# Kernel optimization log

Hardware: AMD Instinct MI355X
Metric: run time of the kernel (lower is better)

Reference implementation:

```python
import jax, jax.numpy as jnp
import numpy as np

IN_DIMS = 512
TOKEN_DIM = 512
NUM_HEADS = 1
D = TOKEN_DIM * NUM_HEADS
SCALE = TOKEN_DIM ** (-0.5)
EPS = 1e-12  # torch F.normalize default


def _l2norm(v, axis):
    n = jnp.sqrt(jnp.sum(v * v, axis=axis, keepdims=True))
    return v / jnp.maximum(n, EPS)


def setup_inputs() -> dict:
    key = jax.random.key(0)
    ks = jax.random.split(key, 10)
    B, C, H, W = 64, IN_DIMS, 28, 28
    s_in = IN_DIMS ** -0.5
    s_d = D ** -0.5
    return {
        "x": jax.random.normal(ks[0], (B, C, H, W), jnp.float32),
        "Wq": jax.random.normal(ks[1], (IN_DIMS, D), jnp.float32) * s_in,
        "bq": jax.random.normal(ks[2], (D,), jnp.float32) * 0.01,
        "Wk": jax.random.normal(ks[3], (IN_DIMS, D), jnp.float32) * s_in,
        "bk": jax.random.normal(ks[4], (D,), jnp.float32) * 0.01,
        "w_g": jax.random.normal(ks[5], (D, 1), jnp.float32),
        "Wp": jax.random.normal(ks[6], (D, D), jnp.float32) * s_d,
        "bp": jax.random.normal(ks[7], (D,), jnp.float32) * 0.01,
        "Wf": jax.random.normal(ks[8], (D, TOKEN_DIM), jnp.float32) * s_d,
        "bf": jax.random.normal(ks[9], (TOKEN_DIM,), jnp.float32) * 0.01,
    }


def reference(x, Wq, bq, Wk, bk, w_g, Wp, bp, Wf, bf):
    B, C, H, W = x.shape
    t = x.reshape(B, C, H * W).transpose(0, 2, 1)          # [B, N, C]
    query = _l2norm(t @ Wq + bq, axis=-1)                  # [B, N, D]
    k = _l2norm(t @ Wk + bk, axis=-1)                      # [B, N, D]
    attn = _l2norm((query @ w_g) * SCALE, axis=1)          # [B, N, 1], normalized over tokens
    ctx = jnp.sum(attn * query, axis=1, keepdims=True)     # [B, 1, D] global context
    out = (ctx * k) @ Wp + bp + query                      # [B, N, D]
    out = out @ Wf + bf                                    # [B, N, TOKEN_DIM]
    return out.transpose(0, 2, 1).reshape(B, -1, H, W)
```

## Files before the change

### kernel.cpp

```cpp
#include <hip/hip_runtime.h>

#define EPSN 1e-12f
#define SCALE_F 0.044194173824159216f

typedef __bf16 bf16x8 __attribute__((ext_vector_type(8)));
typedef __bf16 bf16x4 __attribute__((ext_vector_type(4)));
typedef float  f32x4  __attribute__((ext_vector_type(4)));

__global__ __launch_bounds__(256) void k_prep_t(const float* __restrict__ Wq,
                                                const float* __restrict__ Wk,
                                                __bf16* __restrict__ WqT,
                                                __bf16* __restrict__ WkT) {
  __shared__ float Tq[32][33], Tk[32][33];
  const int c0 = blockIdx.x * 32, d0 = blockIdx.y * 32;
  const int dx = threadIdx.x, cy = threadIdx.y;
  #pragma unroll
  for (int p = 0; p < 4; ++p) {
    int c = cy + p * 8;
    Tq[c][dx] = Wq[(size_t)(c0 + c) * 512 + d0 + dx];
    Tk[c][dx] = Wk[(size_t)(c0 + c) * 512 + d0 + dx];
  }
  __syncthreads();
  #pragma unroll
  for (int p = 0; p < 4; ++p) {
    int d = cy + p * 8;
    WqT[(size_t)(d0 + d) * 512 + c0 + dx] = (__bf16)Tq[dx][d];
    WkT[(size_t)(d0 + d) * 512 + c0 + dx] = (__bf16)Tk[dx][d];
  }
}

__global__ __launch_bounds__(512) void k_prep_w(const float* __restrict__ Wp,
                                                const float* __restrict__ Wf,
                                                const float* __restrict__ bp,
                                                const float* __restrict__ bfv,
                                                __bf16* __restrict__ WcT,
                                                float* __restrict__ bpf) {
  int kk = blockIdx.x;
  int d  = threadIdx.x;
  float a0 = 0.f, a1 = 0.f, a2 = 0.f, a3 = 0.f;
  for (int c = 0; c < 512; c += 4) {
    a0 = fmaf(Wp[kk * 512 + c],     Wf[(size_t)c * 512 + d],         a0);
    a1 = fmaf(Wp[kk * 512 + c + 1], Wf[(size_t)(c + 1) * 512 + d],   a1);
    a2 = fmaf(Wp[kk * 512 + c + 2], Wf[(size_t)(c + 2) * 512 + d],   a2);
    a3 = fmaf(Wp[kk * 512 + c + 3], Wf[(size_t)(c + 3) * 512 + d],   a3);
  }
  WcT[(size_t)d * 1024 + kk]       = (__bf16)((a0 + a1) + (a2 + a3));
  WcT[(size_t)d * 1024 + 512 + kk] = (__bf16)Wf[(size_t)kk * 512 + d];
  if (kk == 0) {
    float b0 = 0.f, b1 = 0.f;
    for (int c = 0; c < 512; c += 2) {
      b0 = fmaf(bp[c],     Wf[(size_t)c * 512 + d],       b0);
      b1 = fmaf(bp[c + 1], Wf[(size_t)(c + 1) * 512 + d], b1);
    }
    bpf[d] = b0 + b1 + bfv[d];
  }
}

__global__ __launch_bounds__(512) void k_qk(const float* __restrict__ x,
                                            const __bf16* __restrict__ WqT,
                                            const __bf16* __restrict__ WkT,
                                            const float* __restrict__ bq,
                                            const float* __restrict__ bk,
                                            const float* __restrict__ wg,
                                            __bf16* __restrict__ Qn,
                                            __bf16* __restrict__ Kn,
                                            float* __restrict__ g) {
  __shared__ __bf16 As0[64][40], As1[64][40];
  __shared__ float red[8][64], redG[8][64];
  __shared__ float invv[64];
  const int t = threadIdx.x;
  const int lane = t & 63, w = t >> 6;
  const int li = lane & 15, lq = lane >> 4;
  const int n0 = blockIdx.x * 64;
  const int b  = blockIdx.y;
  const int isK = blockIdx.z;
  const __bf16* Wt  = isK ? WkT : WqT;
  const float* bias = isK ? bk : bq;
  __bf16* dst       = isK ? Kn : Qn;
  const int sn = t & 63, sc4 = (t >> 6) * 4;
  const bool nv = (n0 + sn < 784);
  const float* xp = x + ((size_t)b * 512 + sc4) * 784 + n0 + sn;
  const __bf16* wp = Wt + (size_t)(w * 64 + li) * 512 + lq * 8;

  f32x4 acc[4][4] = {};
  bf16x8 bA[4], bB[4];
  float xA[4], xB[4];

  auto issueX = [&](float (&xr)[4], int ks) {
    #pragma unroll
    for (int j = 0; j < 4; ++j)
      xr[j] = nv ? xp[(size_t)(ks * 32 + j) * 784] : 0.f;
  };
  auto issueB = [&](bf16x8 (&bb)[4], int ks) {
    #pragma unroll
    for (int cb = 0; cb < 4; ++cb)
      bb[cb] = *(const bf16x8*)(wp + (size_t)cb * 8192 + ks * 32);
  };
  auto writeA = [&](__bf16 (*Asb)[40], const float (&xr)[4]) {
    bf16x4 v;
    #pragma unroll
    for (int j = 0; j < 4; ++j) v[j] = (__bf16)xr[j];
    *(bf16x4*)&Asb[sn][sc4] = v;
  };
  auto step = [&](const __bf16 (*Asb)[40], const bf16x8 (&bb)[4]) {
    bf16x8 af[4];
    #pragma unroll
    for (int rb = 0; rb < 4; ++rb)
      af[rb] = *(const bf16x8*)&Asb[rb * 16 + li][lq * 8];
    #pragma unroll
    for (int cb = 0; cb < 4; ++cb)
      #pragma unroll
      for (int rb = 0; rb < 4; ++rb)
        acc[rb][cb] = __builtin_amdgcn_mfma_f32_16x16x32_bf16(af[rb], bb[cb], acc[rb][cb], 0, 0, 0);
  };

  issueX(xA, 0); issueX(xB, 1); issueB(bA, 0);
  writeA(As0, xA);
  __syncthreads();

  #pragma unroll 1
  for (int ks = 0; ks < 14; ks += 2) {
    issueX(xA, ks + 2);
    issueB(bB, ks + 1);
    step(As0, bA);
    writeA(As1, xB);
    __syncthreads();
    issueX(xB, ks + 3);
    issueB(bA, ks + 2);
    step(As1, bB);
    writeA(As0, xA);
    __syncthreads();
  }
  issueB(bB, 15);
  step(As0, bA);
  writeA(As1, xB);
  __syncthreads();
  step(As1, bB);

  float bv[4], wv[4];
  #pragma unroll
  for (int cb = 0; cb < 4; ++cb) {
    int col = w * 64 + cb * 16 + li;
    bv[cb] = bias[col];
    wv[cb] = isK ? 0.f : wg[col];
  }
  #pragma unroll
  for (int rb = 0; rb < 4; ++rb)
    #pragma unroll
    for (int cb = 0; cb < 4; ++cb)
      #pragma unroll
      for (int j = 0; j < 4; ++j)
        acc[rb][cb][j] += bv[cb];
  #pragma unroll
  for (int rb = 0; rb < 4; ++rb)
    #pragma unroll
    for (int j = 0; j < 4; ++j) {
      float ss = 0.f, sg = 0.f;
      #pragma unroll
      for (int cb = 0; cb < 4; ++cb) {
        float v = acc[rb][cb][j];
        ss = fmaf(v, v, ss); sg = fmaf(v, wv[cb], sg);
      }
      ss += __shfl_xor(ss, 1); ss += __shfl_xor(ss, 2); ss += __shfl_xor(ss, 4); ss += __shfl_xor(ss, 8);
      sg += __shfl_xor(sg, 1); sg += __shfl_xor(sg, 2); sg += __shfl_xor(sg, 4); sg += __shfl_xor(sg, 8);
      if (li == 0) {
        int row = rb * 16 + lq * 4 + j;
        red[w][row] = ss; redG[w][row] = sg;
      }
    }
  __syncthreads();
  if (t < 64) {
    float ss = 0.f, sg = 0.f;
    #pragma unroll
    for (int wv2 = 0; wv2 < 8; ++wv2) { ss += red[wv2][t]; sg += redG[wv2][t]; }
    float iv = 1.f / fmaxf(sqrtf(ss), EPSN);
    invv[t] = iv;
    if (!isK && (n0 + t < 784)) g[(size_t)b * 784 + n0 + t] = sg * iv;
  }
  __syncthreads();
  #pragma unroll
  for (int rb = 0; rb < 4; ++rb)
    #pragma unroll
    for (int j = 0; j < 4; ++j) {
      int row = rb * 16 + lq * 4 + j;
      if (n0 + row < 784) {
        float iv = invv[row];
        size_t base = ((size_t)b * 784 + n0 + row) * 512 + w * 64 + li;
        #pragma unroll
        for (int cb = 0; cb < 4; ++cb)
          dst[base + cb * 16] = (__bf16)(acc[rb][cb][j] * iv);
      }
    }
}

__global__ __launch_bounds__(512) void k_ctx1(const __bf16* __restrict__ Qn,
                                              const float* __restrict__ g,
                                              float* __restrict__ pctx,
                                              float* __restrict__ pgsq) {
  const int cx = blockIdx.x;
  const int b  = blockIdx.y;
  const int t  = threadIdx.x;
  const int nbase = cx * 112;
  __shared__ float wred[8];
  const float* gb = g + (size_t)b * 784 + nbase;
  float s = 0.f;
  if (t < 112) { float v = gb[t]; s = v * v; }
  s += __shfl_xor(s, 1);  s += __shfl_xor(s, 2);  s += __shfl_xor(s, 4);
  s += __shfl_xor(s, 8);  s += __shfl_xor(s, 16); s += __shfl_xor(s, 32);
  if ((t & 63) == 0) wred[t >> 6] = s;
  __syncthreads();
  if (t == 0) {
    float tot = 0.f;
    #pragma unroll
    for (int i = 0; i < 8; ++i) tot += wred[i];
    pgsq[b * 7 + cx] = tot;
  }
  const __bf16* qb = Qn + ((size_t)b * 784 + nbase) * 512 + t;
  float a0 = 0.f, a1 = 0.f, a2 = 0.f, a3 = 0.f;
  for (int n = 0; n < 112; n += 4) {
    a0 = fmaf(gb[n],     (float)qb[(size_t)n * 512],       a0);
    a1 = fmaf(gb[n + 1], (float)qb[(size_t)(n + 1) * 512], a1);
    a2 = fmaf(gb[n + 2], (float)qb[(size_t)(n + 2) * 512], a2);
    a3 = fmaf(gb[n + 3], (float)qb[(size_t)(n + 3) * 512], a3);
  }
  pctx[((size_t)b * 7 + cx) * 512 + t] = (a0 + a1) + (a2 + a3);
}

__global__ __launch_bounds__(512) void k_ctx2(const float* __restrict__ pctx,
                                              const float* __restrict__ pgsq,
                                              float* __restrict__ ctx) {
  const int b = blockIdx.x, t = threadIdx.x;
  float tot = 0.f;
  #pragma unroll
  for (int i = 0; i < 7; ++i) tot += pgsq[b * 7 + i];
  float alpha = SCALE_F / fmaxf(sqrtf(tot) * SCALE_F, EPSN);
  float s = 0.f;
  #pragma unroll
  for (int i = 0; i < 7; ++i) s += pctx[((size_t)b * 7 + i) * 512 + t];
  ctx[(size_t)b * 512 + t] = alpha * s;
}

__global__ __launch_bounds__(512) void k_out(const __bf16* __restrict__ Qn,
                                             const __bf16* __restrict__ Kn,
                                             const float* __restrict__ ctx,
                                             const __bf16* __restrict__ WcT,
                                             const float* __restrict__ bpf,
                                             float* __restrict__ out) {
  __shared__ __bf16 As0[64][40], As1[64][40];
  const int t = threadIdx.x;
  const int lane = t & 63, w = t >> 6;
  const int li = lane & 15, lq = lane >> 4;
  const int n0 = blockIdx.x * 64;
  const int b  = blockIdx.y;
  const int an = t & 63, ak4 = (t >> 6) * 4;
  const bool anv = (n0 + an < 784);
  const __bf16* qrow = Qn + ((size_t)b * 784 + n0 + an) * 512;
  const __bf16* krow = Kn + ((size_t)b * 784 + n0 + an) * 512;
  const float* cxp = ctx + (size_t)b * 512;
  const __bf16* wp = WcT + (size_t)(w * 64 + li) * 1024 + lq * 8;

  f32x4 acc[4][4] = {};
  bf16x8 bA[4], bB[4];
  bf16x4 aA, aB;
  f32x4 cA, cB;

  auto issueA = [&](bf16x4& aq, f32x4& cx, int ks) {
    int kk = ks * 32 + ak4;
    bf16x4 v = {};
    if (ks < 16) {
      if (anv) v = *(const bf16x4*)(krow + kk);
      cx = *(const f32x4*)(cxp + kk);
    } else {
      if (anv) v = *(const bf16x4*)(qrow + kk - 512);
    }
    aq = v;
  };
  auto issueB = [&](bf16x8 (&bb)[4], int ks) {
    #pragma unroll
    for (int cb = 0; cb < 4; ++cb)
      bb[cb] = *(const bf16x8*)(wp + (size_t)cb * 16384 + ks * 32);
  };
  auto writeA = [&](__bf16 (*Asb)[40], bf16x4 aq, f32x4 cx, int ks) {
    bf16x4 v;
    if (ks < 16) {
      #pragma unroll
      for (int j = 0; j < 4; ++j) v[j] = (__bf16)((float)aq[j] * cx[j]);
    } else {
      v = aq;
    }
    *(bf16x4*)&Asb[an][ak4] = v;
  };
  auto step = [&](const __bf16 (*Asb)[40], const bf16x8 (&bb)[4]) {
    bf16x8 af[4];
    #pragma unroll
    for (int rb = 0; rb < 4; ++rb)
      af[rb] = *(const bf16x8*)&Asb[rb * 16 + li][lq * 8];
    #pragma unroll
    for (int cb = 0; cb < 4; ++cb)
      #pragma unroll
      for (int rb = 0; rb < 4; ++rb)
        acc[rb][cb] = __builtin_amdgcn_mfma_f32_16x16x32_bf16(af[rb], bb[cb], acc[rb][cb], 0, 0, 0);
  };

  issueA(aA, cA, 0); issueA(aB, cB, 1); issueB(bA, 0);
  writeA(As0, aA, cA, 0);
  __syncthreads();

  #pragma unroll 1
  for (int ks = 0; ks < 30; ks += 2) {
    issueA(aA, cA, ks + 2);
    issueB(bB, ks + 1);
    step(As0, bA);
    writeA(As1, aB, cB, ks + 1);
    __syncthreads();
    issueA(aB, cB, ks + 3);
    issueB(bA, ks + 2);
    step(As1, bB);
    writeA(As0, aA, cA, ks + 2);
    __syncthreads();
  }
  issueB(bB, 31);
  step(As0, bA);
  writeA(As1, aB, cB, 31);
  __syncthreads();
  step(As1, bB);

  float bv[4];
  #pragma unroll
  for (int cb = 0; cb < 4; ++cb) bv[cb] = bpf[w * 64 + cb * 16 + li];
  #pragma unroll
  for (int rb = 0; rb < 4; ++rb) {
    int nrow = n0 + rb * 16 + lq * 4;
    if (nrow < 784) {
      #pragma unroll
      for (int cb = 0; cb < 4; ++cb) {
        f32x4 v;
        #pragma unroll
        for (int j = 0; j < 4; ++j) v[j] = acc[rb][cb][j] + bv[cb];
        *(f32x4*)&out[((size_t)b * 512 + w * 64 + cb * 16 + li) * 784 + nrow] = v;
      }
    }
  }
}

extern "C" void kernel_launch(void* const* d_in, const int* in_sizes, int n_in,
                              void* d_out, int out_size, void* d_ws, size_t ws_size,
                              hipStream_t stream) {
  const float* x   = (const float*)d_in[0];
  const float* Wq  = (const float*)d_in[1];
  const float* bq  = (const float*)d_in[2];
  const float* Wk  = (const float*)d_in[3];
  const float* bk  = (const float*)d_in[4];
  const float* wg  = (const float*)d_in[5];
  const float* Wp  = (const float*)d_in[6];
  const float* bp  = (const float*)d_in[7];
  const float* Wf  = (const float*)d_in[8];
  const float* bfv = (const float*)d_in[9];
  float* out = (float*)d_out;
  char* ws = (char*)d_ws;

  const size_t SZQN = (size_t)64 * 784 * 512 * 2;
  __bf16* Qn   = (__bf16*)(ws);
  __bf16* Kn   = (__bf16*)(ws + SZQN);
  __bf16* WqT  = (__bf16*)(ws + 2 * SZQN);
  __bf16* WkT  = (__bf16*)(ws + 2 * SZQN + 524288);
  __bf16* WcT  = (__bf16*)(ws + 2 * SZQN + 2 * 524288);
  float*  gbuf = (float*) (ws + 2 * SZQN + 2 * 524288 + 1048576);
  float*  ctx  = (float*) (ws + 2 * SZQN + 2 * 524288 + 1048576 + 200704);
  float*  bpf  = (float*) (ws + 2 * SZQN + 2 * 524288 + 1048576 + 200704 + 131072);
  float*  pctx = (float*)(ws + 2 * SZQN);
  float*  pgsq = (float*)(ws + 2 * SZQN + 917504);

  k_prep_t<<<dim3(16, 16),    dim3(32, 8), 0, stream>>>(Wq, Wk, WqT, WkT);
  k_prep_w<<<dim3(512),       dim3(512),   0, stream>>>(Wp, Wf, bp, bfv, WcT, bpf);
  k_qk    <<<dim3(13, 64, 2), dim3(512),   0, stream>>>(x, WqT, WkT, bq, bk, wg, Qn, Kn, gbuf);
  k_ctx1  <<<dim3(7, 64),     dim3(512),   0, stream>>>(Qn, gbuf, pctx, pgsq);
  k_ctx2  <<<dim3(64),        dim3(512),   0, stream>>>(pctx, pgsq, ctx);
  k_out   <<<dim3(13, 64),    dim3(512),   0, stream>>>(Qn, Kn, ctx, WcT, bpf, out);
}
```

Measured before the change: 400.6 us.

## Fuse Q/K projections into one block and fold context partial sums into epilogue

The QK kernel now loads a 64-token slab of x into shared memory once, converted to bf16, and runs both the Q and K GEMMs against it. Previously a separate grid z-slice reread x for each. The Q pass epilogue computes the gate, its squared partial sum and the per-block context partial sums directly, which removes the k_ctx1 kernel and its reread of Qn. The output kernel likewise stages full 64x512 K*ctx and Q tiles in LDS and runs two full-K loops instead of a double-buffered 32-wide pipeline. The costs are a larger shared-memory footprint (about 66KB), fewer blocks with less inter-block parallelism, and loss of the explicit load/compute overlap.

```diff
diff --git a/kernel.cpp b/kernel.cpp
--- a/kernel.cpp
+++ b/kernel.cpp
@@ -64,166 +64,144 @@
                                             const float* __restrict__ wg,
                                             __bf16* __restrict__ Qn,
                                             __bf16* __restrict__ Kn,
-                                            float* __restrict__ g) {
-  __shared__ __bf16 As0[64][40], As1[64][40];
+                                            float* __restrict__ pctx,
+                                            float* __restrict__ pgsq) {
+  __shared__ __bf16 Xs[64][520];
   __shared__ float red[8][64], redG[8][64];
-  __shared__ float invv[64];
+  __shared__ float invv[64], gs[64];
   const int t = threadIdx.x;
   const int lane = t & 63, w = t >> 6;
   const int li = lane & 15, lq = lane >> 4;
   const int n0 = blockIdx.x * 64;
   const int b  = blockIdx.y;
-  const int isK = blockIdx.z;
-  const __bf16* Wt  = isK ? WkT : WqT;
-  const float* bias = isK ? bk : bq;
-  __bf16* dst       = isK ? Kn : Qn;
   const int sn = t & 63, sc4 = (t >> 6) * 4;
   const bool nv = (n0 + sn < 784);
   const float* xp = x + ((size_t)b * 512 + sc4) * 784 + n0 + sn;
-  const __bf16* wp = Wt + (size_t)(w * 64 + li) * 512 + lq * 8;
-
-  f32x4 acc[4][4] = {};
-  bf16x8 bA[4], bB[4];
-  float xA[4], xB[4];
-
-  auto issueX = [&](float (&xr)[4], int ks) {
-    #pragma unroll
-    for (int j = 0; j < 4; ++j)
-      xr[j] = nv ? xp[(size_t)(ks * 32 + j) * 784] : 0.f;
+
+  #pragma unroll
+  for (int ks = 0; ks < 16; ++ks) {
+    float v0 = nv ? xp[(size_t)(ks * 32 + 0) * 784] : 0.f;
+    float v1 = nv ? xp[(size_t)(ks * 32 + 1) * 784] : 0.f;
+    float v2 = nv ? xp[(size_t)(ks * 32 + 2) * 784] : 0.f;
+    float v3 = nv ? xp[(size_t)(ks * 32 + 3) * 784] : 0.f;
+    bf16x4 v; v[0] = (__bf16)v0; v[1] = (__bf16)v1; v[2] = (__bf16)v2; v[3] = (__bf16)v3;
+    *(bf16x4*)&Xs[sn][ks * 32 + sc4] = v;
+  }
+  __syncthreads();
+
+  auto gemmPass = [&](const __bf16* Wt, const float* bias, bool isQ, __bf16* dst) {
+    const __bf16* wp = Wt + (size_t)(w * 64 + li) * 512 + lq * 8;
+    f32x4 acc[4][4] = {};
+    bf16x8 bA[4], bB[4];
+    #pragma unroll
+    for (int cb = 0; cb < 4; ++cb) bA[cb] = *(const bf16x8*)(wp + cb * 8192);
+    #pragma unroll
+    for (int ks = 0; ks < 16; ks += 2) {
+      #pragma unroll
+      for (int cb = 0; cb < 4; ++cb) bB[cb] = *(const bf16x8*)(wp + cb * 8192 + (ks + 1) * 32);
+      bf16x8 af[4];
+      #pragma unroll
+      for (int rb = 0; rb < 4; ++rb) af[rb] = *(const bf16x8*)&Xs[rb * 16 + li][ks * 32 + lq * 8];
+      #pragma unroll
+      for (int cb = 0; cb < 4; ++cb)
+        #pragma unroll
+        for (int rb = 0; rb < 4; ++rb)
+          acc[rb][cb] = __builtin_amdgcn_mfma_f32_16x16x32_bf16(af[rb], bA[cb], acc[rb][cb], 0, 0, 0);
+      if (ks + 2 < 16) {
+        #pragma unroll
+        for (int cb = 0; cb < 4; ++cb) bA[cb] = *(const bf16x8*)(wp + cb * 8192 + (ks + 2) * 32);
+      }
+      #pragma unroll
+      for (int rb = 0; rb < 4; ++rb) af[rb] = *(const bf16x8*)&Xs[rb * 16 + li][(ks + 1) * 32 + lq * 8];
+      #pragma unroll
+      for (int cb = 0; cb < 4; ++cb)
+        #pragma unroll
+        for (int rb = 0; rb < 4; ++rb)
+          acc[rb][cb] = __builtin_amdgcn_mfma_f32_16x16x32_bf16(af[rb], bB[cb], acc[rb][cb], 0, 0, 0);
+    }
+
+    float bv[4], wv[4];
+    #pragma unroll
+    for (int cb = 0; cb < 4; ++cb) {
+      int col = w * 64 + cb * 16 + li;
+      bv[cb] = bias[col];
+      wv[cb] = isQ ? wg[col] : 0.f;
+    }
+    #pragma unroll
+    for (int rb = 0; rb < 4; ++rb)
+      #pragma unroll
+      for (int cb = 0; cb < 4; ++cb)
+        #pragma unroll
+        for (int j = 0; j < 4; ++j)
+          acc[rb][cb][j] += bv[cb];
+    #pragma unroll
+    for (int rb = 0; rb < 4; ++rb)
+      #pragma unroll
+      for (int j = 0; j < 4; ++j) {
+        float ss = 0.f, sg = 0.f;
+        #pragma unroll
+        for (int cb = 0; cb < 4; ++cb) {
+          float v = acc[rb][cb][j];
+          ss = fmaf(v, v, ss); sg = fmaf(v, wv[cb], sg);
+        }
+        ss += __shfl_xor(ss, 1); ss += __shfl_xor(ss, 2); ss += __shfl_xor(ss, 4); ss += __shfl_xor(ss, 8);
+        sg += __shfl_xor(sg, 1); sg += __shfl_xor(sg, 2); sg += __shfl_xor(sg, 4); sg += __shfl_xor(sg, 8);
+        if (li == 0) {
+          int row = rb * 16 + lq * 4 + j;
+          red[w][row] = ss; redG[w][row] = sg;
+        }
+      }
+    __syncthreads();
+    if (t < 64) {
+      float ss = 0.f, sg = 0.f;
+      #pragma unroll
+      for (int wv2 = 0; wv2 < 8; ++wv2) { ss += red[wv2][t]; sg += redG[wv2][t]; }
+      float iv = 1.f / fmaxf(sqrtf(ss), EPSN);
+      invv[t] = iv;
+      if (isQ) {
+        float gv = (n0 + t < 784) ? sg * iv : 0.f;
+        gs[t] = gv;
+        float pg = gv * gv;
+        pg += __shfl_xor(pg, 1);  pg += __shfl_xor(pg, 2);  pg += __shfl_xor(pg, 4);
+        pg += __shfl_xor(pg, 8);  pg += __shfl_xor(pg, 16); pg += __shfl_xor(pg, 32);
+        if (t == 0) pgsq[b * 13 + blockIdx.x] = pg;
+      }
+    }
+    __syncthreads();
+    float pc[4] = {0.f, 0.f, 0.f, 0.f};
+    #pragma unroll
+    for (int rb = 0; rb < 4; ++rb)
+      #pragma unroll
+      for (int j = 0; j < 4; ++j) {
+        int row = rb * 16 + lq * 4 + j;
+        if (n0 + row < 784) {
+          float iv = invv[row];
+          float gr = isQ ? gs[row] : 0.f;
+          size_t base = ((size_t)b * 784 + n0 + row) * 512 + w * 64 + li;
+          #pragma unroll
+          for (int cb = 0; cb < 4; ++cb) {
+            float qv = acc[rb][cb][j] * iv;
+            dst[base + cb * 16] = (__bf16)qv;
+            pc[cb] = fmaf(gr, qv, pc[cb]);
+          }
+        }
+      }
+    if (isQ) {
+      #pragma unroll
+      for (int cb = 0; cb < 4; ++cb) {
+        pc[cb] += __shfl_xor(pc[cb], 16);
+        pc[cb] += __shfl_xor(pc[cb], 32);
+      }
+      if (lq == 0) {
+        #pragma unroll
+        for (int cb = 0; cb < 4; ++cb)
+          pctx[((size_t)b * 13 + blockIdx.x) * 512 + w * 64 + cb * 16 + li] = pc[cb];
+      }
+    }
   };
-  auto issueB = [&](bf16x8 (&bb)[4], int ks) {
-    #pragma unroll
-    for (int cb = 0; cb < 4; ++cb)
-      bb[cb] = *(const bf16x8*)(wp + (size_t)cb * 8192 + ks * 32);
-  };
-  auto writeA = [&](__bf16 (*Asb)[40], const float (&xr)[4]) {
-    bf16x4 v;
-    #pragma unroll
-    for (int j = 0; j < 4; ++j) v[j] = (__bf16)xr[j];
-    *(bf16x4*)&Asb[sn][sc4] = v;
-  };
-  auto step = [&](const __bf16 (*Asb)[40], const bf16x8 (&bb)[4]) {
-    bf16x8 af[4];
-    #pragma unroll
-    for (int rb = 0; rb < 4; ++rb)
-      af[rb] = *(const bf16x8*)&Asb[rb * 16 + li][lq * 8];
-    #pragma unroll
-    for (int cb = 0; cb < 4; ++cb)
-      #pragma unroll
-      for (int rb = 0; rb < 4; ++rb)
-        acc[rb][cb] = __builtin_amdgcn_mfma_f32_16x16x32_bf16(af[rb], bb[cb], acc[rb][cb], 0, 0, 0);
-  };
-
-  issueX(xA, 0); issueX(xB, 1); issueB(bA, 0);
-  writeA(As0, xA);
-  __syncthreads();
-
-  #pragma unroll 1
-  for (int ks = 0; ks < 14; ks += 2) {
-    issueX(xA, ks + 2);
-    issueB(bB, ks + 1);
-    step(As0, bA);
-    writeA(As1, xB);
-    __syncthreads();
-    issueX(xB, ks + 3);
-    issueB(bA, ks + 2);
-    step(As1, bB);
-    writeA(As0, xA);
-    __syncthreads();
-  }
-  issueB(bB, 15);
-  step(As0, bA);
-  writeA(As1, xB);
-  __syncthreads();
-  step(As1, bB);
-
-  float bv[4], wv[4];
-  #pragma unroll
-  for (int cb = 0; cb < 4; ++cb) {
-    int col = w * 64 + cb * 16 + li;
-    bv[cb] = bias[col];
-    wv[cb] = isK ? 0.f : wg[col];
-  }
-  #pragma unroll
-  for (int rb = 0; rb < 4; ++rb)
-    #pragma unroll
-    for (int cb = 0; cb < 4; ++cb)
-      #pragma unroll
-      for (int j = 0; j < 4; ++j)
-        acc[rb][cb][j] += bv[cb];
-  #pragma unroll
-  for (int rb = 0; rb < 4; ++rb)
-    #pragma unroll
-    for (int j = 0; j < 4; ++j) {
-      float ss = 0.f, sg = 0.f;
-      #pragma unroll
-      for (int cb = 0; cb < 4; ++cb) {
-        float v = acc[rb][cb][j];
-        ss = fmaf(v, v, ss); sg = fmaf(v, wv[cb], sg);
-      }
-      ss += __shfl_xor(ss, 1); ss += __shfl_xor(ss, 2); ss += __shfl_xor(ss, 4); ss += __shfl_xor(ss, 8);
-      sg += __shfl_xor(sg, 1); sg += __shfl_xor(sg, 2); sg += __shfl_xor(sg, 4); sg += __shfl_xor(sg, 8);
-      if (li == 0) {
-        int row = rb * 16 + lq * 4 + j;
-        red[w][row] = ss; redG[w][row] = sg;
-      }
-    }
-  __syncthreads();
-  if (t < 64) {
-    float ss = 0.f, sg = 0.f;
-    #pragma unroll
-    for (int wv2 = 0; wv2 < 8; ++wv2) { ss += red[wv2][t]; sg += redG[wv2][t]; }
-    float iv = 1.f / fmaxf(sqrtf(ss), EPSN);
-    invv[t] = iv;
-    if (!isK && (n0 + t < 784)) g[(size_t)b * 784 + n0 + t] = sg * iv;
-  }
-  __syncthreads();
-  #pragma unroll
-  for (int rb = 0; rb < 4; ++rb)
-    #pragma unroll
-    for (int j = 0; j < 4; ++j) {
-      int row = rb * 16 + lq * 4 + j;
-      if (n0 + row < 784) {
-        float iv = invv[row];
-        size_t base = ((size_t)b * 784 + n0 + row) * 512 + w * 64 + li;
-        #pragma unroll
-        for (int cb = 0; cb < 4; ++cb)
-          dst[base + cb * 16] = (__bf16)(acc[rb][cb][j] * iv);
-      }
-    }
-}
-
-__global__ __launch_bounds__(512) void k_ctx1(const __bf16* __restrict__ Qn,
-                                              const float* __restrict__ g,
-                                              float* __restrict__ pctx,
-                                              float* __restrict__ pgsq) {
-  const int cx = blockIdx.x;
-  const int b  = blockIdx.y;
-  const int t  = threadIdx.x;
-  const int nbase = cx * 112;
-  __shared__ float wred[8];
-  const float* gb = g + (size_t)b * 784 + nbase;
-  float s = 0.f;
-  if (t < 112) { float v = gb[t]; s = v * v; }
-  s += __shfl_xor(s, 1);  s += __shfl_xor(s, 2);  s += __shfl_xor(s, 4);
-  s += __shfl_xor(s, 8);  s += __shfl_xor(s, 16); s += __shfl_xor(s, 32);
-  if ((t & 63) == 0) wred[t >> 6] = s;
-  __syncthreads();
-  if (t == 0) {
-    float tot = 0.f;
-    #pragma unroll
-    for (int i = 0; i < 8; ++i) tot += wred[i];
-    pgsq[b * 7 + cx] = tot;
-  }
-  const __bf16* qb = Qn + ((size_t)b * 784 + nbase) * 512 + t;
-  float a0 = 0.f, a1 = 0.f, a2 = 0.f, a3 = 0.f;
-  for (int n = 0; n < 112; n += 4) {
-    a0 = fmaf(gb[n],     (float)qb[(size_t)n * 512],       a0);
-    a1 = fmaf(gb[n + 1], (float)qb[(size_t)(n + 1) * 512], a1);
-    a2 = fmaf(gb[n + 2], (float)qb[(size_t)(n + 2) * 512], a2);
-    a3 = fmaf(gb[n + 3], (float)qb[(size_t)(n + 3) * 512], a3);
-  }
-  pctx[((size_t)b * 7 + cx) * 512 + t] = (a0 + a1) + (a2 + a3);
+
+  gemmPass(WqT, bq, true,  Qn);
+  gemmPass(WkT, bk, false, Kn);
 }
 
 __global__ __launch_bounds__(512) void k_ctx2(const float* __restrict__ pctx,
@@ -232,11 +210,11 @@
   const int b = blockIdx.x, t = threadIdx.x;
   float tot = 0.f;
   #pragma unroll
-  for (int i = 0; i < 7; ++i) tot += pgsq[b * 7 + i];
+  for (int i = 0; i < 13; ++i) tot += pgsq[b * 13 + i];
   float alpha = SCALE_F / fmaxf(sqrtf(tot) * SCALE_F, EPSN);
   float s = 0.f;
   #pragma unroll
-  for (int i = 0; i < 7; ++i) s += pctx[((size_t)b * 7 + i) * 512 + t];
+  for (int i = 0; i < 13; ++i) s += pctx[((size_t)b * 13 + i) * 512 + t];
   ctx[(size_t)b * 512 + t] = alpha * s;
 }
 
@@ -246,84 +224,74 @@
                                              const __bf16* __restrict__ WcT,
                                              const float* __restrict__ bpf,
                                              float* __restrict__ out) {
-  __shared__ __bf16 As0[64][40], As1[64][40];
+  __shared__ __bf16 Xs[64][520];
   const int t = threadIdx.x;
   const int lane = t & 63, w = t >> 6;
   const int li = lane & 15, lq = lane >> 4;
   const int n0 = blockIdx.x * 64;
   const int b  = blockIdx.y;
-  const int an = t & 63, ak4 = (t >> 6) * 4;
-  const bool anv = (n0 + an < 784);
-  const __bf16* qrow = Qn + ((size_t)b * 784 + n0 + an) * 512;
-  const __bf16* krow = Kn + ((size_t)b * 784 + n0 + an) * 512;
   const float* cxp = ctx + (size_t)b * 512;
-  const __bf16* wp = WcT + (size_t)(w * 64 + li) * 1024 + lq * 8;
 
   f32x4 acc[4][4] = {};
-  bf16x8 bA[4], bB[4];
-  bf16x4 aA, aB;
-  f32x4 cA, cB;
-
-  auto issueA = [&](bf16x4& aq, f32x4& cx, int ks) {
-    int kk = ks * 32 + ak4;
-    bf16x4 v = {};
-    if (ks < 16) {
-      if (anv) v = *(const bf16x4*)(krow + kk);
-      cx = *(const f32x4*)(cxp + kk);
-    } else {
-      if (anv) v = *(const bf16x4*)(qrow + kk - 512);
-    }
-    aq = v;
+
+  auto mloop = [&](const __bf16* wp) {
+    bf16x8 bA[4], bB[4];
+    #pragma unroll
+    for (int cb = 0; cb < 4; ++cb) bA[cb] = *(const bf16x8*)(wp + (size_t)cb * 16384);
+    #pragma unroll
+    for (int ks = 0; ks < 16; ks += 2) {
+      #pragma unroll
+      for (int cb = 0; cb < 4; ++cb) bB[cb] = *(const bf16x8*)(wp + (size_t)cb * 16384 + (ks + 1) * 32);
+      bf16x8 af[4];
+      #pragma unroll
+      for (int rb = 0; rb < 4; ++rb) af[rb] = *(const bf16x8*)&Xs[rb * 16 + li][ks * 32 + lq * 8];
+      #pragma unroll
+      for (int cb = 0; cb < 4; ++cb)
+        #pragma unroll
+        for (int rb = 0; rb < 4; ++rb)
+          acc[rb][cb] = __builtin_amdgcn_mfma_f32_16x16x32_bf16(af[rb], bA[cb], acc[rb][cb], 0, 0, 0);
+      if (ks + 2 < 16) {
+        #pragma unroll
+        for (int cb = 0; cb < 4; ++cb) bA[cb] = *(const bf16x8*)(wp + (size_t)cb * 16384 + (ks + 2) * 32);
+      }
+      #pragma unroll
+      for (int rb = 0; rb < 4; ++rb) af[rb] = *(const bf16x8*)&Xs[rb * 16 + li][(ks + 1) * 32 + lq * 8];
+      #pragma unroll
+      for (int cb = 0; cb < 4; ++cb)
+        #pragma unroll
+        for (int rb = 0; rb < 4; ++rb)
+          acc[rb][cb] = __builtin_amdgcn_mfma_f32_16x16x32_bf16(af[rb], bB[cb], acc[rb][cb], 0, 0, 0);
+    }
   };
-  auto issueB = [&](bf16x8 (&bb)[4], int ks) {
-    #pragma unroll
-    for (int cb = 0; cb < 4; ++cb)
-      bb[cb] = *(const bf16x8*)(wp + (size_t)cb * 16384 + ks * 32);
-  };
-  auto writeA = [&](__bf16 (*Asb)[40], bf16x4 aq, f32x4 cx, int ks) {
-    bf16x4 v;
-    if (ks < 16) {
-      #pragma unroll
-      for (int j = 0; j < 4; ++j) v[j] = (__bf16)((float)aq[j] * cx[j]);
-    } else {
-      v = aq;
-    }
-    *(bf16x4*)&Asb[an][ak4] = v;
-  };
-  auto step = [&](const __bf16 (*Asb)[40], const bf16x8 (&bb)[4]) {
-    bf16x8 af[4];
-    #pragma unroll
-    for (int rb = 0; rb < 4; ++rb)
-      af[rb] = *(const bf16x8*)&Asb[rb * 16 + li][lq * 8];
-    #pragma unroll
-    for (int cb = 0; cb < 4; ++cb)
-      #pragma unroll
-      for (int rb = 0; rb < 4; ++rb)
-        acc[rb][cb] = __builtin_amdgcn_mfma_f32_16x16x32_bf16(af[rb], bb[cb], acc[rb][cb], 0, 0, 0);
-  };
-
-  issueA(aA, cA, 0); issueA(aB, cB, 1); issueB(bA, 0);
-  writeA(As0, aA, cA, 0);
-  __syncthreads();
-
-  #pragma unroll 1
-  for (int ks = 0; ks < 30; ks += 2) {
-    issueA(aA, cA, ks + 2);
-    issueB(bB, ks + 1);
-    step(As0, bA);
-    writeA(As1, aB, cB, ks + 1);
-    __syncthreads();
-    issueA(aB, cB, ks + 3);
-    issueB(bA, ks + 2);
-    step(As1, bB);
-    writeA(As0, aA, cA, ks + 2);
-    __syncthreads();
-  }
-  issueB(bB, 31);
-  step(As0, bA);
-  writeA(As1, aB, cB, 31);
-  __syncthreads();
-  step(As1, bB);
+
+  #pragma unroll
+  for (int p = 0; p < 8; ++p) {
+    int id = t + p * 512, n = id >> 6, c8 = id & 63;
+    bf16x8 v = {};
+    if (n0 + n < 784) v = *(const bf16x8*)(Kn + ((size_t)b * 784 + n0 + n) * 512 + c8 * 8);
+    f32x4 c0 = *(const f32x4*)(cxp + c8 * 8);
+    f32x4 c1 = *(const f32x4*)(cxp + c8 * 8 + 4);
+    bf16x8 r;
+    #pragma unroll
+    for (int j = 0; j < 4; ++j) {
+      r[j]     = (__bf16)((float)v[j]     * c0[j]);
+      r[4 + j] = (__bf16)((float)v[4 + j] * c1[j]);
+    }
+    *(bf16x8*)&Xs[n][c8 * 8] = r;
+  }
+  __syncthreads();
+  mloop(WcT + (size_t)(w * 64 + li) * 1024 + lq * 8);
+  __syncthreads();
+
+  #pragma unroll
+  for (int p = 0; p < 8; ++p) {
+    int id = t + p * 512, n = id >> 6, c8 = id & 63;
+    bf16x8 v = {};
+    if (n0 + n < 784) v = *(const bf16x8*)(Qn + ((size_t)b * 784 + n0 + n) * 512 + c8 * 8);
+    *(bf16x8*)&Xs[n][c8 * 8] = v;
+  }
+  __syncthreads();
+  mloop(WcT + (size_t)(w * 64 + li) * 1024 + 512 + lq * 8);
 
   float bv[4];
   #pragma unroll
@@ -365,16 +333,14 @@
   __bf16* WqT  = (__bf16*)(ws + 2 * SZQN);
   __bf16* WkT  = (__bf16*)(ws + 2 * SZQN + 524288);
   __bf16* WcT  = (__bf16*)(ws + 2 * SZQN + 2 * 524288);
-  float*  gbuf = (float*) (ws + 2 * SZQN + 2 * 524288 + 1048576);
-  float*  ctx  = (float*) (ws + 2 * SZQN + 2 * 524288 + 1048576 + 200704);
-  float*  bpf  = (float*) (ws + 2 * SZQN + 2 * 524288 + 1048576 + 200704 + 131072);
-  float*  pctx = (float*)(ws + 2 * SZQN);
-  float*  pgsq = (float*)(ws + 2 * SZQN + 917504);
-
-  k_prep_t<<<dim3(16, 16),    dim3(32, 8), 0, stream>>>(Wq, Wk, WqT, WkT);
-  k_prep_w<<<dim3(512),       dim3(512),   0, stream>>>(Wp, Wf, bp, bfv, WcT, bpf);
-  k_qk    <<<dim3(13, 64, 2), dim3(512),   0, stream>>>(x, WqT, WkT, bq, bk, wg, Qn, Kn, gbuf);
-  k_ctx1  <<<dim3(7, 64),     dim3(512),   0, stream>>>(Qn, gbuf, pctx, pgsq);
-  k_ctx2  <<<dim3(64),        dim3(512),   0, stream>>>(pctx, pgsq, ctx);
-  k_out   <<<dim3(13, 64),    dim3(512),   0, stream>>>(Qn, Kn, ctx, WcT, bpf, out);
-}
+  float*  bpf  = (float*) (ws + 2 * SZQN + 2 * 524288 + 1048576);
+  float*  pctx = (float*) (ws + 2 * SZQN + 2 * 524288 + 1048576 + 2048);
+  float*  pgsq = (float*) (ws + 2 * SZQN + 2 * 524288 + 1048576 + 2048 + 1703936);
+  float*  ctx  = (float*) (ws + 2 * SZQN + 2 * 524288 + 1048576 + 2048 + 1703936 + 4096);
+
+  k_prep_t<<<dim3(16, 16), dim3(32, 8), 0, stream>>>(Wq, Wk, WqT, WkT);
+  k_prep_w<<<dim3(512),    dim3(512),   0, stream>>>(Wp, Wf, bp, bfv, WcT, bpf);
+  k_qk    <<<dim3(13, 64), dim3(512),   0, stream>>>(x, WqT, WkT, bq, bk, wg, Qn, Kn, pctx, pgsq);
+  k_ctx2  <<<dim3(64),     dim3(512),   0, stream>>>(pctx, pgsq, ctx);
+  k_out   <<<dim3(13, 64), dim3(512),   0, stream>>>(Qn, Kn, ctx, WcT, bpf, out);
+}
```

Result: slower. 477.6 us (+19.2%).
